# Kernel optimization log

Hardware: AMD Instinct MI355X
Metric: run time of the kernel (lower is better)

## Reference

```python
import jax, jax.numpy as jnp
import numpy as np
import math

N_EMB = 768
N_HEAD = 12
N_INNER = 3072
B, T = 2, 2048
EPS = 1e-4


def _gelu_tanh(x):
    return x * 0.5 * (1.0 + jnp.tanh(math.sqrt(2.0 / math.pi) * (x + 0.044715 * x ** 3)))


def _layernorm(x, scale, bias):
    mean = jnp.mean(x, axis=-1, keepdims=True)
    var = jnp.var(x, axis=-1, keepdims=True, ddof=1)  # torch.var default: unbiased
    return scale * ((x - mean) / jnp.sqrt(var + EPS)) + bias


def setup_inputs() -> dict:
    key = jax.random.key(0)
    ks = jax.random.split(key, 16)
    s_attn = 1.0 / math.sqrt(N_EMB)
    s_mlp1 = 1.0 / math.sqrt(N_EMB)
    s_mlp2 = 1.0 / math.sqrt(N_INNER)
    return {
        "x": jax.random.normal(ks[0], (B, T, N_EMB), dtype=jnp.float32),
        "Wq": jax.random.normal(ks[1], (N_EMB, N_EMB), dtype=jnp.float32) * s_attn,
        "bq": jnp.zeros((N_EMB,), jnp.float32),
        "Wk": jax.random.normal(ks[2], (N_EMB, N_EMB), dtype=jnp.float32) * s_attn,
        "bk": jnp.zeros((N_EMB,), jnp.float32),
        "Wv": jax.random.normal(ks[3], (N_EMB, N_EMB), dtype=jnp.float32) * s_attn,
        "bv": jnp.zeros((N_EMB,), jnp.float32),
        "Wo": jax.random.normal(ks[4], (N_EMB, N_EMB), dtype=jnp.float32) * s_attn,
        "bo": jnp.zeros((N_EMB,), jnp.float32),
        "ln1_s": jnp.ones((N_EMB,), jnp.float32),
        "ln1_b": jnp.zeros((N_EMB,), jnp.float32),
        "W1": jax.random.normal(ks[5], (N_EMB, N_INNER), dtype=jnp.float32) * s_mlp1,
        "b1": jnp.zeros((N_INNER,), jnp.float32),
        "W2": jax.random.normal(ks[6], (N_INNER, N_EMB), dtype=jnp.float32) * s_mlp2,
        "b2": jnp.zeros((N_EMB,), jnp.float32),
        "ln2_s": jnp.ones((N_EMB,), jnp.float32),
        "ln2_b": jnp.zeros((N_EMB,), jnp.float32),
    }


def reference(x, Wq, bq, Wk, bk, Wv, bv, Wo, bo, ln1_s, ln1_b, W1, b1, W2, b2, ln2_s, ln2_b):
    Bx, Tx, C = x.shape
    dh = C // N_HEAD
    # QKV projections -> [B, H, T, dh]
    def split_heads(y):
        return y.reshape(Bx, Tx, N_HEAD, dh).transpose(0, 2, 1, 3)
    q = split_heads(x @ Wq + bq)
    k = split_heads(x @ Wk + bk)
    v = split_heads(x @ Wv + bv)
    # naive full-score causal attention (materializes [B,H,T,T])
    scores = jnp.einsum("bhqd,bhkd->bhqk", q, k)
    causal = jnp.tril(jnp.ones((Tx, Tx), dtype=bool))
    scores = jnp.where(causal, scores, -jnp.inf)
    attn = jax.nn.softmax(scores / math.sqrt(dh), axis=-1)
    ctx = jnp.einsum("bhqk,bhkd->bhqd", attn, v)
    ctx = ctx.transpose(0, 2, 1, 3).reshape(Bx, Tx, C)
    attn_out = ctx @ Wo + bo
    # post-norm residual
    h = _layernorm(x + attn_out, ln1_s, ln1_b)
    mlp_out = _gelu_tanh(h @ W1 + b1) @ W2 + b2
    return _layernorm(h + mlp_out, ln2_s, ln2_b)
```

## Files before the change

kernel.cpp:

```cpp
#include <hip/hip_runtime.h>
#include <math.h>

#define TB  2
#define TT  2048
#define TC  768
#define TH  12
#define TDH 64
#define TI  3072
#define TM  (TB*TT)

typedef __attribute__((ext_vector_type(8))) __bf16 bf16x8;
typedef __attribute__((ext_vector_type(4))) __bf16 bf16x4;
typedef __attribute__((ext_vector_type(4))) float  f32x4;

__device__ __forceinline__ float gelu_tanh(float x) {
    float x3 = x * x * x;
    return 0.5f * x * (1.0f + tanhf(0.7978845608028654f * (x + 0.044715f * x3)));
}

__device__ __forceinline__ void gld_lds16(const void* g, void* l) {
    __builtin_amdgcn_global_load_lds(
        (const __attribute__((address_space(1))) unsigned int*)g,
        (__attribute__((address_space(3))) unsigned int*)l,
        16, 0, 0);
}

#define BK 32

template<int BM_, int BN_, int WM_, int WN_>
__global__ __launch_bounds__(256)
void gemm_mfma(const __bf16* __restrict__ A, const __bf16* __restrict__ Bt,
               const float* __restrict__ b0, const float* __restrict__ b1,
               const float* __restrict__ b2, const float* __restrict__ resid,
               float* __restrict__ outf, __bf16* __restrict__ outb,
               int N, int K, size_t wt_stride, size_t out_stride, int ep)
{
    constexpr int WAVES_N = BN_ / WN_;
    constexpr int TMt = WM_ / 16, TNt = WN_ / 16;
    constexpr int AISS = BM_ / 64, BISS = BN_ / 64;
    constexpr int TILE = (BM_ + BN_) * BK;
    __shared__ __align__(16) __bf16 lds[2 * TILE];

    const int tid  = threadIdx.x;
    const int wave = tid >> 6, lane = tid & 63;
    const int wm = wave / WAVES_N, wn = wave % WAVES_N;
    const int m0 = blockIdx.y * BM_, n0 = blockIdx.x * BN_;
    const int z  = blockIdx.z;

    const __bf16* Bz = Bt + (size_t)z * wt_stride;
    const size_t Kb = (size_t)K * 2;
    const char* Ag = (const char*)A + (size_t)m0 * Kb;
    const char* Bg = (const char*)Bz + (size_t)n0 * Kb;
    const int srow = tid >> 2;
    const int scol = ((tid & 3) ^ ((tid >> 4) & 3)) * 16;
    const int wbase = wave * 1024;

    f32x4 acc[TMt][TNt];
    #pragma unroll
    for (int i = 0; i < TMt; ++i)
        #pragma unroll
        for (int j = 0; j < TNt; ++j)
            acc[i][j] = (f32x4){0.f, 0.f, 0.f, 0.f};

    const int arow = wm * WM_ + (lane & 15);
    const int brow = wn * WN_ + (lane & 15);
    const int koff = (((lane >> 4) ^ ((lane >> 2) & 3))) * 8;

    const int nIter = K / BK;

    auto stage = [&](int buf, int k0b) {
        char* base = (char*)lds + (size_t)buf * TILE * 2;
        #pragma unroll
        for (int s = 0; s < AISS; ++s)
            gld_lds16(Ag + (size_t)(srow + 64 * s) * Kb + k0b + scol,
                      base + s * 4096 + wbase);
        char* bbase = base + BM_ * BK * 2;
        #pragma unroll
        for (int s = 0; s < BISS; ++s)
            gld_lds16(Bg + (size_t)(srow + 64 * s) * Kb + k0b + scol,
                      bbase + s * 4096 + wbase);
    };

    stage(0, 0);
    int buf = 0;
    for (int it = 0; it < nIter; ++it) {
        __syncthreads();
        if (it + 1 < nIter) stage(buf ^ 1, (it + 1) * (BK * 2));

        const __bf16* As = lds + (size_t)buf * TILE;
        const __bf16* Bs = As + BM_ * BK;
        bf16x8 af[TMt], bfr[TNt];
        #pragma unroll
        for (int ti = 0; ti < TMt; ++ti)
            af[ti] = *(const bf16x8*)&As[(arow + ti * 16) * BK + koff];
        #pragma unroll
        for (int tj = 0; tj < TNt; ++tj)
            bfr[tj] = *(const bf16x8*)&Bs[(brow + tj * 16) * BK + koff];
        #pragma unroll
        for (int ti = 0; ti < TMt; ++ti)
            #pragma unroll
            for (int tj = 0; tj < TNt; ++tj)
                acc[ti][tj] = __builtin_amdgcn_mfma_f32_16x16x32_bf16(
                    af[ti], bfr[tj], acc[ti][tj], 0, 0, 0);
        buf ^= 1;
    }

    const int lrow = m0 + wm * WM_ + ((lane >> 4) << 2);
    const int lcol = n0 + wn * WN_ + (lane & 15);

    if (ep == 0) {
        const float* bias = (z == 0) ? b0 : (z == 1) ? b1 : b2;
        __bf16* outz = outb + (size_t)z * out_stride;
        if (z < 2) {
            #pragma unroll
            for (int tj = 0; tj < TNt; ++tj) {
                int n = lcol + tj * 16;
                float bj = bias[n];
                int h = n >> 6, d = n & 63;
                #pragma unroll
                for (int ti = 0; ti < TMt; ++ti)
                    #pragma unroll
                    for (int r = 0; r < 4; ++r) {
                        int m = lrow + ti * 16 + r;
                        int b = m >> 11, t = m & (TT - 1);
                        outz[((size_t)(b * TH + h) * TT + t) * TDH + d] =
                            (__bf16)(acc[ti][tj][r] + bj);
                    }
            }
        } else {
            #pragma unroll
            for (int tj = 0; tj < TNt; ++tj) {
                int n = lcol + tj * 16;
                float bj = bias[n];
                int h = n >> 6, d = n & 63;
                #pragma unroll
                for (int ti = 0; ti < TMt; ++ti) {
                    int m = lrow + ti * 16;
                    int b = m >> 11, t0 = m & (TT - 1);
                    bf16x4 pk;
                    #pragma unroll
                    for (int r = 0; r < 4; ++r)
                        pk[r] = (__bf16)(acc[ti][tj][r] + bj);
                    *(bf16x4*)(outz + ((size_t)(b * TH + h) * TDH + d) * TT + t0) = pk;
                }
            }
        }
    } else if (ep == 1) {
        #pragma unroll
        for (int tj = 0; tj < TNt; ++tj) {
            int n = lcol + tj * 16;
            float bj = b0[n];
            #pragma unroll
            for (int ti = 0; ti < TMt; ++ti)
                #pragma unroll
                for (int r = 0; r < 4; ++r) {
                    int m = lrow + ti * 16 + r;
                    outf[(size_t)m * N + n] =
                        acc[ti][tj][r] + bj + resid[(size_t)m * N + n];
                }
        }
    } else {
        #pragma unroll
        for (int tj = 0; tj < TNt; ++tj) {
            int n = lcol + tj * 16;
            float bj = b0[n];
            #pragma unroll
            for (int ti = 0; ti < TMt; ++ti)
                #pragma unroll
                for (int r = 0; r < 4; ++r) {
                    int m = lrow + ti * 16 + r;
                    outb[(size_t)m * N + n] = (__bf16)gelu_tanh(acc[ti][tj][r] + bj);
                }
        }
    }
}

__global__ __launch_bounds__(256)
void prep_kernel(const float* __restrict__ x,
                 const float* __restrict__ Wq, const float* __restrict__ Wk,
                 const float* __restrict__ Wv, const float* __restrict__ Wo,
                 const float* __restrict__ W1, const float* __restrict__ W2,
                 __bf16* __restrict__ x_bf, __bf16* __restrict__ WqkvT,
                 __bf16* __restrict__ WoT, __bf16* __restrict__ W1T,
                 __bf16* __restrict__ W2T)
{
    const size_t WSZ = (size_t)TC * TC;
    int bid = blockIdx.x;
    if (bid < 1536) {
        int i = (bid * 256 + threadIdx.x) * 8;
        float4 a = *(const float4*)(x + i);
        float4 b = *(const float4*)(x + i + 4);
        bf16x8 v;
        v[0] = (__bf16)a.x; v[1] = (__bf16)a.y; v[2] = (__bf16)a.z; v[3] = (__bf16)a.w;
        v[4] = (__bf16)b.x; v[5] = (__bf16)b.y; v[6] = (__bf16)b.z; v[7] = (__bf16)b.w;
        *(bf16x8*)(x_bf + i) = v;
        return;
    }
    bid -= 1536;
    const float* src; __bf16* dst; int K, N, tloc;
    if (bid < 2304) {
        int w = bid / 576; tloc = bid - w * 576;
        K = TC; N = TC;
        src = (w == 0) ? Wq : (w == 1) ? Wk : (w == 2) ? Wv : Wo;
        dst = (w < 3) ? (WqkvT + (size_t)w * WSZ) : WoT;
    } else if (bid < 4608) {
        tloc = bid - 2304; K = TC; N = TI; src = W1; dst = W1T;
    } else {
        tloc = bid - 4608; K = TI; N = TC; src = W2; dst = W2T;
    }
    int tiles_x = N >> 5;
    int n0 = (tloc % tiles_x) * 32, k0 = (tloc / tiles_x) * 32;

    __shared__ float tile[32][33];
    const int tx = threadIdx.x & 31, ty = threadIdx.x >> 5;
    #pragma unroll
    for (int i = 0; i < 32; i += 8)
        tile[ty + i][tx] = src[(size_t)(k0 + ty + i) * N + n0 + tx];
    __syncthreads();
    #pragma unroll
    for (int i = 0; i < 32; i += 8)
        dst[(size_t)(n0 + ty + i) * K + k0 + tx] = (__bf16)tile[tx][ty + i];
}

__global__ __launch_bounds__(256)
void ln_kernel(const float* __restrict__ in, const float* __restrict__ gs,
               const float* __restrict__ gb, float* __restrict__ out,
               __bf16* __restrict__ out_bf)
{
    const int row = blockIdx.x, tid = threadIdx.x;
    const float* r = in + (size_t)row * TC;
    float x0 = r[tid], x1 = r[tid + 256], x2 = r[tid + 512];
    float s = x0 + x1 + x2;
    float q = x0 * x0 + x1 * x1 + x2 * x2;
    #pragma unroll
    for (int off = 32; off > 0; off >>= 1) {
        s += __shfl_down(s, off);
        q += __shfl_down(q, off);
    }
    __shared__ float partial[8];
    __shared__ float stats[2];
    int wid = tid >> 6, lane = tid & 63;
    if (lane == 0) { partial[wid] = s; partial[wid + 4] = q; }
    __syncthreads();
    if (tid == 0) {
        float S = partial[0] + partial[1] + partial[2] + partial[3];
        float Q = partial[4] + partial[5] + partial[6] + partial[7];
        float mean = S * (1.0f / (float)TC);
        float var = (Q - (float)TC * mean * mean) * (1.0f / (float)(TC - 1));
        stats[0] = mean;
        stats[1] = rsqrtf(var + 1e-4f);
    }
    __syncthreads();
    float mean = stats[0], rstd = stats[1];
    float* w = out + (size_t)row * TC;
    float y0 = gs[tid]       * ((x0 - mean) * rstd) + gb[tid];
    float y1 = gs[tid + 256] * ((x1 - mean) * rstd) + gb[tid + 256];
    float y2 = gs[tid + 512] * ((x2 - mean) * rstd) + gb[tid + 512];
    w[tid] = y0; w[tid + 256] = y1; w[tid + 512] = y2;
    if (out_bf) {
        __bf16* wb = out_bf + (size_t)row * TC;
        wb[tid] = (__bf16)y0; wb[tid + 256] = (__bf16)y1; wb[tid + 512] = (__bf16)y2;
    }
}

#define AP 72

__global__ __launch_bounds__(256)
void attn_mfma(const __bf16* __restrict__ Q, const __bf16* __restrict__ K,
               const __bf16* __restrict__ Vt, __bf16* __restrict__ ctx)
{
    __shared__ __align__(16) __bf16 Ks[64 * AP];
    __shared__ __align__(16) __bf16 Vs[64 * AP];
    __shared__ __align__(16) __bf16 Ps[64 * AP];

    const int tid  = threadIdx.x;
    const int wave = tid >> 6, lane = tid & 63;
    const int c = lane & 15, g = lane >> 4;
    const int bh = blockIdx.y;
    const int qi = blockIdx.x;
    const int qt = (qi & 1) ? (31 - (qi >> 1)) : (qi >> 1);
    const int q_glob = qt * 64 + wave * 16 + c;

    const __bf16* Qb = Q  + (size_t)bh * TT * TDH;
    const __bf16* Kb = K  + (size_t)bh * TT * TDH;
    const __bf16* Vb = Vt + (size_t)bh * TDH * TT;

    bf16x8 qf0 = *(const bf16x8*)(Qb + (size_t)q_glob * TDH + g * 8);
    bf16x8 qf1 = *(const bf16x8*)(Qb + (size_t)q_glob * TDH + 32 + g * 8);

    const int srow = tid >> 3;
    const int sc   = (tid & 7) * 8;

    float m_i = -1e30f, l_i = 0.0f;
    f32x4 acc[4];
    #pragma unroll
    for (int m2 = 0; m2 < 4; ++m2) acc[m2] = (f32x4){0.f, 0.f, 0.f, 0.f};

    for (int kt = 0; kt <= qt; ++kt) {
        bf16x8 kv0 = *(const bf16x8*)(Kb + (size_t)(kt * 64 + srow) * TDH + sc);
        bf16x8 kv1 = *(const bf16x8*)(Kb + (size_t)(kt * 64 + srow + 32) * TDH + sc);
        bf16x8 vv0 = *(const bf16x8*)(Vb + (size_t)srow * TT + kt * 64 + sc);
        bf16x8 vv1 = *(const bf16x8*)(Vb + (size_t)(srow + 32) * TT + kt * 64 + sc);
        __syncthreads();
        *(bf16x8*)&Ks[srow * AP + sc]        = kv0;
        *(bf16x8*)&Ks[(srow + 32) * AP + sc] = kv1;
        *(bf16x8*)&Vs[srow * AP + sc]        = vv0;
        *(bf16x8*)&Vs[(srow + 32) * AP + sc] = vv1;
        __syncthreads();

        f32x4 st[4];
        #pragma unroll
        for (int g2 = 0; g2 < 4; ++g2) {
            bf16x8 af0 = *(const bf16x8*)&Ks[(16 * g2 + c) * AP + g * 8];
            bf16x8 af1 = *(const bf16x8*)&Ks[(16 * g2 + c) * AP + 32 + g * 8];
            f32x4 z = (f32x4){0.f, 0.f, 0.f, 0.f};
            z = __builtin_amdgcn_mfma_f32_16x16x32_bf16(af0, qf0, z, 0, 0, 0);
            z = __builtin_amdgcn_mfma_f32_16x16x32_bf16(af1, qf1, z, 0, 0, 0);
            st[g2] = z;
        }

        float sv[4][4];
        float mx = -1e30f;
        if (kt == qt) {
            #pragma unroll
            for (int g2 = 0; g2 < 4; ++g2)
                #pragma unroll
                for (int r = 0; r < 4; ++r) {
                    int kcol = kt * 64 + 16 * g2 + 4 * g + r;
                    float v = (kcol > q_glob) ? -1e30f : st[g2][r] * 0.125f;
                    sv[g2][r] = v;
                    mx = fmaxf(mx, v);
                }
        } else {
            #pragma unroll
            for (int g2 = 0; g2 < 4; ++g2)
                #pragma unroll
                for (int r = 0; r < 4; ++r) {
                    float v = st[g2][r] * 0.125f;
                    sv[g2][r] = v;
                    mx = fmaxf(mx, v);
                }
        }
        mx = fmaxf(mx, __shfl_xor(mx, 16));
        mx = fmaxf(mx, __shfl_xor(mx, 32));
        float nm = fmaxf(m_i, mx);
        float corr = __expf(m_i - nm);
        float ps = 0.f;
        #pragma unroll
        for (int g2 = 0; g2 < 4; ++g2) {
            bf16x4 pk;
            #pragma unroll
            for (int r = 0; r < 4; ++r) {
                float p = __expf(sv[g2][r] - nm);
                ps += p;
                pk[r] = (__bf16)p;
            }
            *(bf16x4*)&Ps[(wave * 16 + c) * AP + 16 * g2 + 4 * g] = pk;
        }
        ps += __shfl_xor(ps, 16);
        ps += __shfl_xor(ps, 32);
        l_i = l_i * corr + ps;
        m_i = nm;
        #pragma unroll
        for (int m2 = 0; m2 < 4; ++m2) {
            acc[m2][0] *= corr; acc[m2][1] *= corr;
            acc[m2][2] *= corr; acc[m2][3] *= corr;
        }

        bf16x8 pf0 = *(const bf16x8*)&Ps[(wave * 16 + c) * AP + g * 8];
        bf16x8 pf1 = *(const bf16x8*)&Ps[(wave * 16 + c) * AP + 32 + g * 8];
        #pragma unroll
        for (int m2 = 0; m2 < 4; ++m2) {
            bf16x8 vf0 = *(const bf16x8*)&Vs[(16 * m2 + c) * AP + g * 8];
            bf16x8 vf1 = *(const bf16x8*)&Vs[(16 * m2 + c) * AP + 32 + g * 8];
            acc[m2] = __builtin_amdgcn_mfma_f32_16x16x32_bf16(vf0, pf0, acc[m2], 0, 0, 0);
            acc[m2] = __builtin_amdgcn_mfma_f32_16x16x32_bf16(vf1, pf1, acc[m2], 0, 0, 0);
        }
    }

    const int b = bh / TH, h = bh - b * TH;
    float inv = 1.0f / l_i;
    #pragma unroll
    for (int m2 = 0; m2 < 4; ++m2) {
        bf16x4 o;
        #pragma unroll
        for (int r = 0; r < 4; ++r)
            o[r] = (__bf16)(acc[m2][r] * inv);
        *(bf16x4*)(ctx + ((size_t)b * TT + q_glob) * TC + h * TDH + 16 * m2 + 4 * g) = o;
    }
}

extern "C" void kernel_launch(void* const* d_in, const int* in_sizes, int n_in,
                              void* d_out, int out_size, void* d_ws, size_t ws_size,
                              hipStream_t stream)
{
    const float* x    = (const float*)d_in[0];
    const float* Wq   = (const float*)d_in[1];
    const float* bq   = (const float*)d_in[2];
    const float* Wk   = (const float*)d_in[3];
    const float* bk   = (const float*)d_in[4];
    const float* Wv   = (const float*)d_in[5];
    const float* bv   = (const float*)d_in[6];
    const float* Wo   = (const float*)d_in[7];
    const float* bo   = (const float*)d_in[8];
    const float* ln1s = (const float*)d_in[9];
    const float* ln1b = (const float*)d_in[10];
    const float* W1   = (const float*)d_in[11];
    const float* b1   = (const float*)d_in[12];
    const float* W2   = (const float*)d_in[13];
    const float* b2   = (const float*)d_in[14];
    const float* ln2s = (const float*)d_in[15];
    const float* ln2b = (const float*)d_in[16];
    float* out = (float*)d_out;

    const size_t MC  = (size_t)TM * TC;
    const size_t MCB = MC * 2;
    const size_t WSZ = (size_t)TC * TC;
    const size_t W12 = (size_t)TC * TI;

    char* W = (char*)d_ws;
    __bf16* qkvb  = (__bf16*)W;
    __bf16* x_bf  = (__bf16*)(W + 3 * MCB);
    float*  tmp1  = (float*)W;
    __bf16* u_bf  = (__bf16*)W;
    float*  h_f32 = (float*)(W + 4 * MCB);
    __bf16* ctxh  = (__bf16*)(W + 6 * MCB);
    __bf16* wts   = (__bf16*)(W + 7 * MCB);
    __bf16* WqkvT = wts;
    __bf16* WoT   = WqkvT + 3 * WSZ;
    __bf16* W1T   = WoT + WSZ;
    __bf16* W2T   = W1T + W12;

    dim3 blk(256);

    prep_kernel<<<dim3(1536 + 6912), blk, 0, stream>>>(
        x, Wq, Wk, Wv, Wo, W1, W2, x_bf, WqkvT, WoT, W1T, W2T);

    gemm_mfma<128, 128, 64, 64><<<dim3(TC / 128, TM / 128, 3), blk, 0, stream>>>(
        x_bf, WqkvT, bq, bk, bv, nullptr, nullptr, qkvb, TC, TC, WSZ, MC, 0);

    attn_mfma<<<dim3(TT / 64, TB * TH), blk, 0, stream>>>(
        qkvb, qkvb + MC, qkvb + 2 * MC, ctxh);

    gemm_mfma<64, 128, 32, 64><<<dim3(TC / 128, TM / 64, 1), blk, 0, stream>>>(
        ctxh, WoT, bo, nullptr, nullptr, x, tmp1, nullptr, TC, TC, 0, 0, 1);

    ln_kernel<<<dim3(TM), blk, 0, stream>>>(tmp1, ln1s, ln1b, h_f32, ctxh);

    gemm_mfma<128, 128, 64, 64><<<dim3(TI / 128, TM / 128, 1), blk, 0, stream>>>(
        ctxh, W1T, b1, nullptr, nullptr, nullptr, nullptr, u_bf, TI, TC, 0, 0, 2);

    gemm_mfma<64, 128, 32, 64><<<dim3(TC / 128, TM / 64, 1), blk, 0, stream>>>(
        u_bf, W2T, b2, nullptr, nullptr, h_f32, out, nullptr, TC, TI, 0, 0, 1);

    ln_kernel<<<dim3(TM), blk, 0, stream>>>(out, ln2s, ln2b, out, nullptr);
}
```

Before: 322.6 us.

## Widen attention key tile to 128 and prefetch next K/V tile into registers

The attention kernel now processes 128 keys per loop iteration instead of 64, which halves the number of barrier-separated iterations and uses longer MFMA chains for the score and PV products. The K/V tile for the next iteration is loaded into registers while the current tile is being computed, so global load latency overlaps with MFMA work. In exchange it uses more shared memory and registers, which may lower occupancy. For even query tiles the diagonal step also computes up to half a tile of keys that are then masked away.

```diff
diff --git a/kernel.cpp b/kernel.cpp
--- a/kernel.cpp
+++ b/kernel.cpp
@@ -263,15 +263,16 @@
     }
 }
 
-#define AP 72
+#define KP 72
+#define VP 136
 
 __global__ __launch_bounds__(256)
 void attn_mfma(const __bf16* __restrict__ Q, const __bf16* __restrict__ K,
                const __bf16* __restrict__ Vt, __bf16* __restrict__ ctx)
 {
-    __shared__ __align__(16) __bf16 Ks[64 * AP];
-    __shared__ __align__(16) __bf16 Vs[64 * AP];
-    __shared__ __align__(16) __bf16 Ps[64 * AP];
+    __shared__ __align__(16) __bf16 Ks[128 * KP];
+    __shared__ __align__(16) __bf16 Vs[64 * VP];
+    __shared__ __align__(16) __bf16 Ps[64 * VP];
 
     const int tid  = threadIdx.x;
     const int wave = tid >> 6, lane = tid & 63;
@@ -288,56 +289,78 @@
     bf16x8 qf0 = *(const bf16x8*)(Qb + (size_t)q_glob * TDH + g * 8);
     bf16x8 qf1 = *(const bf16x8*)(Qb + (size_t)q_glob * TDH + 32 + g * 8);
 
-    const int srow = tid >> 3;
-    const int sc   = (tid & 7) * 8;
+    const int kr = tid >> 3;
+    const int kc = (tid & 7) * 8;
+    const int vr = tid >> 4;
+    const int vc = (tid & 15) * 8;
+
+    const int nIter = (qt + 2) >> 1;
+
+    bf16x8 kpre[4], vpre[4];
+    {
+        #pragma unroll
+        for (int s = 0; s < 4; ++s)
+            kpre[s] = *(const bf16x8*)(Kb + (size_t)(s * 32 + kr) * TDH + kc);
+        #pragma unroll
+        for (int s = 0; s < 4; ++s)
+            vpre[s] = *(const bf16x8*)(Vb + (size_t)(s * 16 + vr) * TT + vc);
+    }
 
     float m_i = -1e30f, l_i = 0.0f;
     f32x4 acc[4];
     #pragma unroll
     for (int m2 = 0; m2 < 4; ++m2) acc[m2] = (f32x4){0.f, 0.f, 0.f, 0.f};
 
-    for (int kt = 0; kt <= qt; ++kt) {
-        bf16x8 kv0 = *(const bf16x8*)(Kb + (size_t)(kt * 64 + srow) * TDH + sc);
-        bf16x8 kv1 = *(const bf16x8*)(Kb + (size_t)(kt * 64 + srow + 32) * TDH + sc);
-        bf16x8 vv0 = *(const bf16x8*)(Vb + (size_t)srow * TT + kt * 64 + sc);
-        bf16x8 vv1 = *(const bf16x8*)(Vb + (size_t)(srow + 32) * TT + kt * 64 + sc);
+    for (int it = 0; it < nIter; ++it) {
         __syncthreads();
-        *(bf16x8*)&Ks[srow * AP + sc]        = kv0;
-        *(bf16x8*)&Ks[(srow + 32) * AP + sc] = kv1;
-        *(bf16x8*)&Vs[srow * AP + sc]        = vv0;
-        *(bf16x8*)&Vs[(srow + 32) * AP + sc] = vv1;
+        #pragma unroll
+        for (int s = 0; s < 4; ++s)
+            *(bf16x8*)&Ks[(s * 32 + kr) * KP + kc] = kpre[s];
+        #pragma unroll
+        for (int s = 0; s < 4; ++s)
+            *(bf16x8*)&Vs[(s * 16 + vr) * VP + vc] = vpre[s];
         __syncthreads();
 
-        f32x4 st[4];
-        #pragma unroll
-        for (int g2 = 0; g2 < 4; ++g2) {
-            bf16x8 af0 = *(const bf16x8*)&Ks[(16 * g2 + c) * AP + g * 8];
-            bf16x8 af1 = *(const bf16x8*)&Ks[(16 * g2 + c) * AP + 32 + g * 8];
+        if (it + 1 < nIter) {
+            int kt0 = (it + 1) * 128;
+            #pragma unroll
+            for (int s = 0; s < 4; ++s)
+                kpre[s] = *(const bf16x8*)(Kb + (size_t)(kt0 + s * 32 + kr) * TDH + kc);
+            #pragma unroll
+            for (int s = 0; s < 4; ++s)
+                vpre[s] = *(const bf16x8*)(Vb + (size_t)(s * 16 + vr) * TT + kt0 + vc);
+        }
+
+        f32x4 st[8];
+        #pragma unroll
+        for (int g2 = 0; g2 < 8; ++g2) {
+            bf16x8 af0 = *(const bf16x8*)&Ks[(16 * g2 + c) * KP + g * 8];
+            bf16x8 af1 = *(const bf16x8*)&Ks[(16 * g2 + c) * KP + 32 + g * 8];
             f32x4 z = (f32x4){0.f, 0.f, 0.f, 0.f};
             z = __builtin_amdgcn_mfma_f32_16x16x32_bf16(af0, qf0, z, 0, 0, 0);
             z = __builtin_amdgcn_mfma_f32_16x16x32_bf16(af1, qf1, z, 0, 0, 0);
             st[g2] = z;
         }
 
-        float sv[4][4];
         float mx = -1e30f;
-        if (kt == qt) {
-            #pragma unroll
-            for (int g2 = 0; g2 < 4; ++g2)
+        if (it == nIter - 1) {
+            const int kbase = it * 128;
+            #pragma unroll
+            for (int g2 = 0; g2 < 8; ++g2)
                 #pragma unroll
                 for (int r = 0; r < 4; ++r) {
-                    int kcol = kt * 64 + 16 * g2 + 4 * g + r;
+                    int kcol = kbase + 16 * g2 + 4 * g + r;
                     float v = (kcol > q_glob) ? -1e30f : st[g2][r] * 0.125f;
-                    sv[g2][r] = v;
+                    st[g2][r] = v;
                     mx = fmaxf(mx, v);
                 }
         } else {
             #pragma unroll
-            for (int g2 = 0; g2 < 4; ++g2)
+            for (int g2 = 0; g2 < 8; ++g2)
                 #pragma unroll
                 for (int r = 0; r < 4; ++r) {
                     float v = st[g2][r] * 0.125f;
-                    sv[g2][r] = v;
+                    st[g2][r] = v;
                     mx = fmaxf(mx, v);
                 }
         }
@@ -347,15 +370,15 @@
         float corr = __expf(m_i - nm);
         float ps = 0.f;
         #pragma unroll
-        for (int g2 = 0; g2 < 4; ++g2) {
+        for (int g2 = 0; g2 < 8; ++g2) {
             bf16x4 pk;
             #pragma unroll
             for (int r = 0; r < 4; ++r) {
-                float p = __expf(sv[g2][r] - nm);
+                float p = __expf(st[g2][r] - nm);
                 ps += p;
                 pk[r] = (__bf16)p;
             }
-            *(bf16x4*)&Ps[(wave * 16 + c) * AP + 16 * g2 + 4 * g] = pk;
+            *(bf16x4*)&Ps[(wave * 16 + c) * VP + 16 * g2 + 4 * g] = pk;
         }
         ps += __shfl_xor(ps, 16);
         ps += __shfl_xor(ps, 32);
@@ -367,14 +390,17 @@
             acc[m2][2] *= corr; acc[m2][3] *= corr;
         }
 
-        bf16x8 pf0 = *(const bf16x8*)&Ps[(wave * 16 + c) * AP + g * 8];
-        bf16x8 pf1 = *(const bf16x8*)&Ps[(wave * 16 + c) * AP + 32 + g * 8];
+        bf16x8 pf[4];
+        #pragma unroll
+        for (int ck = 0; ck < 4; ++ck)
+            pf[ck] = *(const bf16x8*)&Ps[(wave * 16 + c) * VP + ck * 32 + g * 8];
         #pragma unroll
         for (int m2 = 0; m2 < 4; ++m2) {
-            bf16x8 vf0 = *(const bf16x8*)&Vs[(16 * m2 + c) * AP + g * 8];
-            bf16x8 vf1 = *(const bf16x8*)&Vs[(16 * m2 + c) * AP + 32 + g * 8];
-            acc[m2] = __builtin_amdgcn_mfma_f32_16x16x32_bf16(vf0, pf0, acc[m2], 0, 0, 0);
-            acc[m2] = __builtin_amdgcn_mfma_f32_16x16x32_bf16(vf1, pf1, acc[m2], 0, 0, 0);
+            #pragma unroll
+            for (int ck = 0; ck < 4; ++ck) {
+                bf16x8 vf = *(const bf16x8*)&Vs[(16 * m2 + c) * VP + ck * 32 + g * 8];
+                acc[m2] = __builtin_amdgcn_mfma_f32_16x16x32_bf16(vf, pf[ck], acc[m2], 0, 0, 0);
+            }
         }
     }
 
```

After: 329.1 us. 1.02x slower.

## Double-buffer attention K/V tiles and split-K the output projection with fused LN reduction

Applied to the files above, without the earlier changes.

The attention kernel now prefetches the next K/V tile into registers and writes it into alternating LDS buffers. This removes one barrier per key tile and overlaps global loads with compute. The Wo projection GEMM is split along K into two partial-sum passes, doubling the block count, and a new fused layernorm kernel adds the two partials, bias and residual before normalising. The trade is extra LDS in attention plus an extra fp32 partial buffer written and read by the fused layernorm.

```diff
diff --git a/kernel.cpp b/kernel.cpp
--- a/kernel.cpp
+++ b/kernel.cpp
@@ -33,7 +33,8 @@
                const float* __restrict__ b0, const float* __restrict__ b1,
                const float* __restrict__ b2, const float* __restrict__ resid,
                float* __restrict__ outf, __bf16* __restrict__ outb,
-               int N, int K, size_t wt_stride, size_t out_stride, int ep)
+               int N, int K, int Kstride, size_t wt_stride, size_t out_stride,
+               int ep)
 {
     constexpr int WAVES_N = BN_ / WN_;
     constexpr int TMt = WM_ / 16, TNt = WN_ / 16;
@@ -48,9 +49,10 @@
     const int z  = blockIdx.z;
 
     const __bf16* Bz = Bt + (size_t)z * wt_stride;
-    const size_t Kb = (size_t)K * 2;
-    const char* Ag = (const char*)A + (size_t)m0 * Kb;
-    const char* Bg = (const char*)Bz + (size_t)n0 * Kb;
+    const size_t Ksb = (size_t)Kstride * 2;
+    const size_t kbaseB = (ep == 3) ? (size_t)z * K * 2 : 0;
+    const char* Ag = (const char*)A + (size_t)m0 * Ksb + kbaseB;
+    const char* Bg = (const char*)Bz + (size_t)n0 * Ksb + kbaseB;
     const int srow = tid >> 2;
     const int scol = ((tid & 3) ^ ((tid >> 4) & 3)) * 16;
     const int wbase = wave * 1024;
@@ -72,12 +74,12 @@
         char* base = (char*)lds + (size_t)buf * TILE * 2;
         #pragma unroll
         for (int s = 0; s < AISS; ++s)
-            gld_lds16(Ag + (size_t)(srow + 64 * s) * Kb + k0b + scol,
+            gld_lds16(Ag + (size_t)(srow + 64 * s) * Ksb + k0b + scol,
                       base + s * 4096 + wbase);
         char* bbase = base + BM_ * BK * 2;
         #pragma unroll
         for (int s = 0; s < BISS; ++s)
-            gld_lds16(Bg + (size_t)(srow + 64 * s) * Kb + k0b + scol,
+            gld_lds16(Bg + (size_t)(srow + 64 * s) * Ksb + k0b + scol,
                       bbase + s * 4096 + wbase);
     };
 
@@ -159,7 +161,7 @@
                         acc[ti][tj][r] + bj + resid[(size_t)m * N + n];
                 }
         }
-    } else {
+    } else if (ep == 2) {
         #pragma unroll
         for (int tj = 0; tj < TNt; ++tj) {
             int n = lcol + tj * 16;
@@ -170,6 +172,19 @@
                 for (int r = 0; r < 4; ++r) {
                     int m = lrow + ti * 16 + r;
                     outb[(size_t)m * N + n] = (__bf16)gelu_tanh(acc[ti][tj][r] + bj);
+                }
+        }
+    } else {
+        float* outz = outf + (size_t)z * out_stride;
+        #pragma unroll
+        for (int tj = 0; tj < TNt; ++tj) {
+            int n = lcol + tj * 16;
+            #pragma unroll
+            for (int ti = 0; ti < TMt; ++ti)
+                #pragma unroll
+                for (int r = 0; r < 4; ++r) {
+                    int m = lrow + ti * 16 + r;
+                    outz[(size_t)m * N + n] = acc[ti][tj][r];
                 }
         }
     }
@@ -222,14 +237,10 @@
         dst[(size_t)(n0 + ty + i) * K + k0 + tx] = (__bf16)tile[tx][ty + i];
 }
 
-__global__ __launch_bounds__(256)
-void ln_kernel(const float* __restrict__ in, const float* __restrict__ gs,
-               const float* __restrict__ gb, float* __restrict__ out,
-               __bf16* __restrict__ out_bf)
-{
-    const int row = blockIdx.x, tid = threadIdx.x;
-    const float* r = in + (size_t)row * TC;
-    float x0 = r[tid], x1 = r[tid + 256], x2 = r[tid + 512];
+__device__ __forceinline__ void ln_core(float x0, float x1, float x2,
+                                        const float* gs, const float* gb,
+                                        float* out_row, __bf16* outbf_row, int tid)
+{
     float s = x0 + x1 + x2;
     float q = x0 * x0 + x1 * x1 + x2 * x2;
     #pragma unroll
@@ -252,15 +263,41 @@
     }
     __syncthreads();
     float mean = stats[0], rstd = stats[1];
-    float* w = out + (size_t)row * TC;
     float y0 = gs[tid]       * ((x0 - mean) * rstd) + gb[tid];
     float y1 = gs[tid + 256] * ((x1 - mean) * rstd) + gb[tid + 256];
     float y2 = gs[tid + 512] * ((x2 - mean) * rstd) + gb[tid + 512];
-    w[tid] = y0; w[tid + 256] = y1; w[tid + 512] = y2;
-    if (out_bf) {
-        __bf16* wb = out_bf + (size_t)row * TC;
-        wb[tid] = (__bf16)y0; wb[tid + 256] = (__bf16)y1; wb[tid + 512] = (__bf16)y2;
-    }
+    out_row[tid] = y0; out_row[tid + 256] = y1; out_row[tid + 512] = y2;
+    if (outbf_row) {
+        outbf_row[tid] = (__bf16)y0;
+        outbf_row[tid + 256] = (__bf16)y1;
+        outbf_row[tid + 512] = (__bf16)y2;
+    }
+}
+
+__global__ __launch_bounds__(256)
+void ln_kernel(const float* __restrict__ in, const float* __restrict__ gs,
+               const float* __restrict__ gb, float* __restrict__ out,
+               __bf16* __restrict__ out_bf)
+{
+    const int row = blockIdx.x, tid = threadIdx.x;
+    const float* r = in + (size_t)row * TC;
+    ln_core(r[tid], r[tid + 256], r[tid + 512], gs, gb,
+            out + (size_t)row * TC,
+            out_bf ? out_bf + (size_t)row * TC : nullptr, tid);
+}
+
+__global__ __launch_bounds__(256)
+void ln_fuse(const float* __restrict__ p0, const float* __restrict__ p1,
+             const float* __restrict__ bias, const float* __restrict__ resid,
+             const float* __restrict__ gs, const float* __restrict__ gb,
+             float* __restrict__ out, __bf16* __restrict__ out_bf)
+{
+    const int row = blockIdx.x, tid = threadIdx.x;
+    const size_t o = (size_t)row * TC;
+    float x0 = p0[o + tid]       + p1[o + tid]       + bias[tid]       + resid[o + tid];
+    float x1 = p0[o + tid + 256] + p1[o + tid + 256] + bias[tid + 256] + resid[o + tid + 256];
+    float x2 = p0[o + tid + 512] + p1[o + tid + 512] + bias[tid + 512] + resid[o + tid + 512];
+    ln_core(x0, x1, x2, gs, gb, out + o, out_bf ? out_bf + o : nullptr, tid);
 }
 
 #define AP 72
@@ -269,8 +306,8 @@
 void attn_mfma(const __bf16* __restrict__ Q, const __bf16* __restrict__ K,
                const __bf16* __restrict__ Vt, __bf16* __restrict__ ctx)
 {
-    __shared__ __align__(16) __bf16 Ks[64 * AP];
-    __shared__ __align__(16) __bf16 Vs[64 * AP];
+    __shared__ __align__(16) __bf16 Ks[2][64 * AP];
+    __shared__ __align__(16) __bf16 Vs[2][64 * AP];
     __shared__ __align__(16) __bf16 Ps[64 * AP];
 
     const int tid  = threadIdx.x;
@@ -288,8 +325,13 @@
     bf16x8 qf0 = *(const bf16x8*)(Qb + (size_t)q_glob * TDH + g * 8);
     bf16x8 qf1 = *(const bf16x8*)(Qb + (size_t)q_glob * TDH + 32 + g * 8);
 
-    const int srow = tid >> 3;
-    const int sc   = (tid & 7) * 8;
+    const int sr = tid >> 3;
+    const int sc = (tid & 7) * 8;
+
+    bf16x8 k0 = *(const bf16x8*)(Kb + (size_t)sr * TDH + sc);
+    bf16x8 k1 = *(const bf16x8*)(Kb + (size_t)(sr + 32) * TDH + sc);
+    bf16x8 v0 = *(const bf16x8*)(Vb + (size_t)sr * TT + sc);
+    bf16x8 v1 = *(const bf16x8*)(Vb + (size_t)(sr + 32) * TT + sc);
 
     float m_i = -1e30f, l_i = 0.0f;
     f32x4 acc[4];
@@ -297,29 +339,31 @@
     for (int m2 = 0; m2 < 4; ++m2) acc[m2] = (f32x4){0.f, 0.f, 0.f, 0.f};
 
     for (int kt = 0; kt <= qt; ++kt) {
-        bf16x8 kv0 = *(const bf16x8*)(Kb + (size_t)(kt * 64 + srow) * TDH + sc);
-        bf16x8 kv1 = *(const bf16x8*)(Kb + (size_t)(kt * 64 + srow + 32) * TDH + sc);
-        bf16x8 vv0 = *(const bf16x8*)(Vb + (size_t)srow * TT + kt * 64 + sc);
-        bf16x8 vv1 = *(const bf16x8*)(Vb + (size_t)(srow + 32) * TT + kt * 64 + sc);
+        const int b = kt & 1;
+        *(bf16x8*)&Ks[b][sr * AP + sc]        = k0;
+        *(bf16x8*)&Ks[b][(sr + 32) * AP + sc] = k1;
+        *(bf16x8*)&Vs[b][sr * AP + sc]        = v0;
+        *(bf16x8*)&Vs[b][(sr + 32) * AP + sc] = v1;
+        if (kt < qt) {
+            const int o = (kt + 1) * 64;
+            k0 = *(const bf16x8*)(Kb + (size_t)(o + sr) * TDH + sc);
+            k1 = *(const bf16x8*)(Kb + (size_t)(o + sr + 32) * TDH + sc);
+            v0 = *(const bf16x8*)(Vb + (size_t)sr * TT + o + sc);
+            v1 = *(const bf16x8*)(Vb + (size_t)(sr + 32) * TT + o + sc);
+        }
         __syncthreads();
-        *(bf16x8*)&Ks[srow * AP + sc]        = kv0;
-        *(bf16x8*)&Ks[(srow + 32) * AP + sc] = kv1;
-        *(bf16x8*)&Vs[srow * AP + sc]        = vv0;
-        *(bf16x8*)&Vs[(srow + 32) * AP + sc] = vv1;
-        __syncthreads();
 
         f32x4 st[4];
         #pragma unroll
         for (int g2 = 0; g2 < 4; ++g2) {
-            bf16x8 af0 = *(const bf16x8*)&Ks[(16 * g2 + c) * AP + g * 8];
-            bf16x8 af1 = *(const bf16x8*)&Ks[(16 * g2 + c) * AP + 32 + g * 8];
+            bf16x8 af0 = *(const bf16x8*)&Ks[b][(16 * g2 + c) * AP + g * 8];
+            bf16x8 af1 = *(const bf16x8*)&Ks[b][(16 * g2 + c) * AP + 32 + g * 8];
             f32x4 z = (f32x4){0.f, 0.f, 0.f, 0.f};
             z = __builtin_amdgcn_mfma_f32_16x16x32_bf16(af0, qf0, z, 0, 0, 0);
             z = __builtin_amdgcn_mfma_f32_16x16x32_bf16(af1, qf1, z, 0, 0, 0);
             st[g2] = z;
         }
 
-        float sv[4][4];
         float mx = -1e30f;
         if (kt == qt) {
             #pragma unroll
@@ -328,7 +372,7 @@
                 for (int r = 0; r < 4; ++r) {
                     int kcol = kt * 64 + 16 * g2 + 4 * g + r;
                     float v = (kcol > q_glob) ? -1e30f : st[g2][r] * 0.125f;
-                    sv[g2][r] = v;
+                    st[g2][r] = v;
                     mx = fmaxf(mx, v);
                 }
         } else {
@@ -337,7 +381,7 @@
                 #pragma unroll
                 for (int r = 0; r < 4; ++r) {
                     float v = st[g2][r] * 0.125f;
-                    sv[g2][r] = v;
+                    st[g2][r] = v;
                     mx = fmaxf(mx, v);
                 }
         }
@@ -351,7 +395,7 @@
             bf16x4 pk;
             #pragma unroll
             for (int r = 0; r < 4; ++r) {
-                float p = __expf(sv[g2][r] - nm);
+                float p = __expf(st[g2][r] - nm);
                 ps += p;
                 pk[r] = (__bf16)p;
             }
@@ -371,8 +415,8 @@
         bf16x8 pf1 = *(const bf16x8*)&Ps[(wave * 16 + c) * AP + 32 + g * 8];
         #pragma unroll
         for (int m2 = 0; m2 < 4; ++m2) {
-            bf16x8 vf0 = *(const bf16x8*)&Vs[(16 * m2 + c) * AP + g * 8];
-            bf16x8 vf1 = *(const bf16x8*)&Vs[(16 * m2 + c) * AP + 32 + g * 8];
+            bf16x8 vf0 = *(const bf16x8*)&Vs[b][(16 * m2 + c) * AP + g * 8];
+            bf16x8 vf1 = *(const bf16x8*)&Vs[b][(16 * m2 + c) * AP + 32 + g * 8];
             acc[m2] = __builtin_amdgcn_mfma_f32_16x16x32_bf16(vf0, pf0, acc[m2], 0, 0, 0);
             acc[m2] = __builtin_amdgcn_mfma_f32_16x16x32_bf16(vf1, pf1, acc[m2], 0, 0, 0);
         }
@@ -421,7 +465,7 @@
     char* W = (char*)d_ws;
     __bf16* qkvb  = (__bf16*)W;
     __bf16* x_bf  = (__bf16*)(W + 3 * MCB);
-    float*  tmp1  = (float*)W;
+    float*  part0 = (float*)W;
     __bf16* u_bf  = (__bf16*)W;
     float*  h_f32 = (float*)(W + 4 * MCB);
     __bf16* ctxh  = (__bf16*)(W + 6 * MCB);
@@ -437,21 +481,23 @@
         x, Wq, Wk, Wv, Wo, W1, W2, x_bf, WqkvT, WoT, W1T, W2T);
 
     gemm_mfma<128, 128, 64, 64><<<dim3(TC / 128, TM / 128, 3), blk, 0, stream>>>(
-        x_bf, WqkvT, bq, bk, bv, nullptr, nullptr, qkvb, TC, TC, WSZ, MC, 0);
+        x_bf, WqkvT, bq, bk, bv, nullptr, nullptr, qkvb, TC, TC, TC, WSZ, MC, 0);
 
     attn_mfma<<<dim3(TT / 64, TB * TH), blk, 0, stream>>>(
         qkvb, qkvb + MC, qkvb + 2 * MC, ctxh);
 
+    gemm_mfma<64, 128, 32, 64><<<dim3(TC / 128, TM / 64, 2), blk, 0, stream>>>(
+        ctxh, WoT, nullptr, nullptr, nullptr, nullptr, part0, nullptr,
+        TC, TC / 2, TC, 0, MC, 3);
+
+    ln_fuse<<<dim3(TM), blk, 0, stream>>>(
+        part0, part0 + MC, bo, x, ln1s, ln1b, h_f32, ctxh);
+
+    gemm_mfma<128, 128, 64, 64><<<dim3(TI / 128, TM / 128, 1), blk, 0, stream>>>(
+        ctxh, W1T, b1, nullptr, nullptr, nullptr, nullptr, u_bf, TI, TC, TC, 0, 0, 2);
+
     gemm_mfma<64, 128, 32, 64><<<dim3(TC / 128, TM / 64, 1), blk, 0, stream>>>(
-        ctxh, WoT, bo, nullptr, nullptr, x, tmp1, nullptr, TC, TC, 0, 0, 1);
-
-    ln_kernel<<<dim3(TM), blk, 0, stream>>>(tmp1, ln1s, ln1b, h_f32, ctxh);
-
-    gemm_mfma<128, 128, 64, 64><<<dim3(TI / 128, TM / 128, 1), blk, 0, stream>>>(
-        ctxh, W1T, b1, nullptr, nullptr, nullptr, nullptr, u_bf, TI, TC, 0, 0, 2);
-
-    gemm_mfma<64, 128, 32, 64><<<dim3(TC / 128, TM / 64, 1), blk, 0, stream>>>(
-        u_bf, W2T, b2, nullptr, nullptr, h_f32, out, nullptr, TC, TI, 0, 0, 1);
+        u_bf, W2T, b2, nullptr, nullptr, h_f32, out, nullptr, TC, TI, TI, 0, 0, 1);
 
     ln_kernel<<<dim3(TM), blk, 0, stream>>>(out, ln2s, ln2b, out, nullptr);
 }
```

Result: no change. 324.6 us (+0.6%).
